# Performance work log

Hardware: AMD Instinct MI355X
Metric: run time of the kernel (lower is better)

## Reference

```python
import jax, jax.numpy as jnp
import numpy as np

EMBED = 1024
HEADS = 16
HEAD_DIM = EMBED // HEADS
WINDOW = 1024
HALF = WINDOW // 2  # effective causal lookback per token is HALF (window positions > i are masked)
SCALE = HEAD_DIM ** -0.5
B, T = 2, 4096


def setup_inputs() -> dict:
    key = jax.random.key(0)
    ks = jax.random.split(key, 11)
    f = jnp.float32
    return {
        'query': jax.random.normal(ks[0], (B, T, EMBED), f),
        'key':   jax.random.normal(ks[1], (B, T, EMBED), f),
        'value': jax.random.normal(ks[2], (B, T, EMBED), f),
        'wq': jax.random.normal(ks[3], (EMBED, EMBED), f) * 0.02,
        'bq': jax.random.normal(ks[4], (EMBED,), f) * 0.02,
        'wk': jax.random.normal(ks[5], (EMBED, EMBED), f) * 0.02,
        'bk': jax.random.normal(ks[6], (EMBED,), f) * 0.02,
        'wv': jax.random.normal(ks[7], (EMBED, EMBED), f) * 0.02,
        'bv': jax.random.normal(ks[8], (EMBED,), f) * 0.02,
        'wo': jax.random.normal(ks[9], (EMBED, EMBED), f) * 0.02,
        'bo': jax.random.normal(ks[10], (EMBED,), f) * 0.02,
    }


def _sliding_window_attn(q, k, v):
    # q,k,v: [B,H,T,D]; each query i attends to keys j with i-HALF <= j <= i.
    # Blocked formulation with block size Bk=HALF: block b attends to blocks b-1 and b.
    Bq, H, Tq, D = q.shape
    Bk = HALF
    nb = Tq // Bk  # T chosen to be a multiple of HALF
    qb = q.reshape(Bq, H, nb, Bk, D)

    def ctx(x):
        xb = x.reshape(Bq, H, nb, Bk, D)
        prev = jnp.concatenate([jnp.zeros_like(xb[:, :, :1]), xb[:, :, :-1]], axis=2)
        return jnp.concatenate([prev, xb], axis=3)  # [B,H,nb,2Bk,D]

    kc, vc = ctx(k), ctx(v)
    scores = jnp.einsum('bhnrd,bhncd->bhnrc', qb, kc)  # [B,H,nb,Bk,2Bk]
    r = jnp.arange(Bk)[:, None]          # query pos within block
    c = jnp.arange(2 * Bk)[None, :]      # key pos within [prev|cur] context
    # global diff = (Bk + r) - c; valid iff 0 <= diff <= HALF  <=>  r <= c <= r + Bk
    band = (c >= r) & (c <= r + Bk)      # [Bk, 2Bk]
    b_idx = jnp.arange(nb)[:, None, None]
    valid = band[None] & ((b_idx > 0) | (c[None] >= Bk))  # first block has no prev keys
    neg_inf = jnp.finfo(jnp.float32).min
    scores = jnp.where(valid[None, None], scores.astype(jnp.float32), neg_inf)
    attn = jax.nn.softmax(scores, axis=-1).astype(q.dtype)
    out = jnp.einsum('bhnrc,bhncd->bhnrd', attn, vc)
    return out.reshape(Bq, H, Tq, D)


def reference(query, key, value, wq, bq, wk, bk, wv, bv, wo, bo):
    Bq, Tq, C = query.shape
    split = lambda x: x.reshape(Bq, Tq, HEADS, HEAD_DIM).transpose(0, 2, 1, 3)
    q = split(jnp.einsum('btc,oc->bto', query, wq) + bq) * SCALE
    k = split(jnp.einsum('btc,oc->bto', key, wk) + bk)
    v = split(jnp.einsum('btc,oc->bto', value, wv) + bv)
    o = _sliding_window_attn(q, k, v)                       # [B,H,T,D]
    o = o.transpose(0, 2, 1, 3).reshape(Bq, Tq, C)
    return jnp.einsum('btc,oc->bto', o, wo) + bo
```

## Files before the change

### kernel.cpp

```cpp
#include <hip/hip_runtime.h>
#include <hip/hip_bf16.h>

typedef __attribute__((ext_vector_type(8))) short short8;
typedef __attribute__((ext_vector_type(4))) float f32x4;

__device__ __forceinline__ unsigned short f2bf(float f) {
  union { float f; unsigned int u; } x; x.f = f;
  unsigned int r = x.u + 0x7fffu + ((x.u >> 16) & 1u);
  return (unsigned short)(r >> 16);
}

__device__ __forceinline__ float fexp2(float x) {
#if __has_builtin(__builtin_amdgcn_exp2f)
  return __builtin_amdgcn_exp2f(x);
#else
  float r;
  asm("v_exp_f32 %0, %1" : "=v"(r) : "v"(x));
  return r;
#endif
}

#define MFMA16(a, b, c) __builtin_amdgcn_mfma_f32_16x16x32_bf16((a), (b), (c), 0, 0, 0)

__device__ __forceinline__ void gload_lds16(const void* g, void* l) {
  __builtin_amdgcn_global_load_lds((const __attribute__((address_space(1))) void*)g,
                                   (__attribute__((address_space(3))) void*)l, 16, 0, 0);
}

#define WAIT_VM(n) asm volatile("s_waitcnt vmcnt(" #n ")" ::: "memory")
#define RAW_BAR() asm volatile("s_barrier" ::: "memory")

__device__ __forceinline__ void p32swap(unsigned int& a, unsigned int& b) {
  asm volatile("v_permlane32_swap_b32 %0, %1" : "+v"(a), "+v"(b));
}
__device__ __forceinline__ void p16swap(unsigned int& a, unsigned int& b) {
  asm volatile("v_permlane16_swap_b32 %0, %1" : "+v"(a), "+v"(b));
}

#define QSCALE 0.1803368801111244f

__global__ __launch_bounds__(256) void cvt8(const float* __restrict__ in,
                                            unsigned short* __restrict__ out, int n8) {
  int i = blockIdx.x * 256 + threadIdx.x;
  if (i >= n8) return;
  const float4* p = (const float4*)in + 2 * (size_t)i;
  float4 a = p[0], b = p[1];
  ushort4 lo, hi;
  lo.x = f2bf(a.x); lo.y = f2bf(a.y); lo.z = f2bf(a.z); lo.w = f2bf(a.w);
  hi.x = f2bf(b.x); hi.y = f2bf(b.y); hi.z = f2bf(b.z); hi.w = f2bf(b.w);
  ((ushort4*)out)[2 * (size_t)i] = lo;
  ((ushort4*)out)[2 * (size_t)i + 1] = hi;
}

__global__ __launch_bounds__(256) void cvt_w(const float* __restrict__ w0,
                                             const float* __restrict__ w1,
                                             const float* __restrict__ w2,
                                             const float* __restrict__ w3,
                                             unsigned short* __restrict__ out) {
  const float* src = (blockIdx.y == 0) ? w0 : (blockIdx.y == 1) ? w1
                     : (blockIdx.y == 2) ? w2 : w3;
  unsigned short* o = out + ((size_t)blockIdx.y << 20);
  const int i = blockIdx.x * 256 + threadIdx.x;
  const float4* p = (const float4*)src + 2 * (size_t)i;
  float4 a = p[0], b = p[1];
  ushort4 lo, hi;
  lo.x = f2bf(a.x); lo.y = f2bf(a.y); lo.z = f2bf(a.z); lo.w = f2bf(a.w);
  hi.x = f2bf(b.x); hi.y = f2bf(b.y); hi.z = f2bf(b.z); hi.w = f2bf(b.w);
  ((ushort4*)o)[2 * (size_t)i] = lo;
  ((ushort4*)o)[2 * (size_t)i + 1] = hi;
}

template <int MODE>
__global__ __launch_bounds__(512) void proj_gemm(const unsigned short* __restrict__ A,
                                                 const unsigned short* __restrict__ W,
                                                 const float* __restrict__ bias,
                                                 void* __restrict__ outp) {
  __shared__ unsigned short As[2][128 * 64];
  __shared__ unsigned short Bs[2][128 * 64];
  const int tid = threadIdx.x, lane = tid & 63, wid = tid >> 6;
  const int g = lane >> 4, li = lane & 15;
  const int wr = wid >> 1, wc = wid & 1;
  const int bm = blockIdx.y, bn = blockIdx.x;
  const int trow = tid >> 3;
  const int js = (tid & 7) ^ (trow & 7);

  f32x4 acc[2][4] = {};

  auto stage = [&](int kt, int pb) {
    const int k0 = kt << 6;
    #pragma unroll
    for (int r = 0; r < 2; ++r) {
      const int row = r * 64 + trow;
      gload_lds16(A + (size_t)(bm * 128 + row) * 1024 + k0 + js * 8,
                  &As[pb][(r * 64 + wid * 8) * 64]);
      gload_lds16(W + (size_t)(bn * 128 + row) * 1024 + k0 + js * 8,
                  &Bs[pb][(r * 64 + wid * 8) * 64]);
    }
  };

  stage(0, 0);
  int p = 0;
  for (int kt = 0; kt < 16; ++kt) {
    if (kt < 15) {
      stage(kt + 1, p ^ 1);
      WAIT_VM(4);
    } else {
      WAIT_VM(0);
    }
    RAW_BAR();
    #pragma unroll
    for (int kst = 0; kst < 2; ++kst) {
      short8 a[2], b[4];
      #pragma unroll
      for (int mi = 0; mi < 2; ++mi) {
        const int row = wr * 32 + mi * 16 + li;
        a[mi] = *(const short8*)((const char*)&As[p][0] + row * 128 +
                                 (((kst * 4 + g) ^ (li & 7)) << 4));
      }
      #pragma unroll
      for (int ni = 0; ni < 4; ++ni) {
        const int row = wc * 64 + ni * 16 + li;
        b[ni] = *(const short8*)((const char*)&Bs[p][0] + row * 128 +
                                 (((kst * 4 + g) ^ (li & 7)) << 4));
      }
      __builtin_amdgcn_s_setprio(1);
      #pragma unroll
      for (int mi = 0; mi < 2; ++mi)
        #pragma unroll
        for (int ni = 0; ni < 4; ++ni) {
          if constexpr (MODE == 2)
            acc[mi][ni] = MFMA16(b[ni], a[mi], acc[mi][ni]);
          else
            acc[mi][ni] = MFMA16(a[mi], b[ni], acc[mi][ni]);
        }
      __builtin_amdgcn_s_setprio(0);
    }
    RAW_BAR();
    p ^= 1;
  }

  #pragma unroll
  for (int mi = 0; mi < 2; ++mi) {
    #pragma unroll
    for (int ni = 0; ni < 4; ++ni) {
      if constexpr (MODE == 2) {
        const int mm = bm * 128 + wr * 32 + mi * 16 + li;
        const int b_ = mm >> 12, t_ = mm & 4095;
        #pragma unroll
        for (int r = 0; r < 4; ++r) {
          const int nn = bn * 128 + wc * 64 + ni * 16 + g * 4 + r;
          const int h_ = nn >> 6, d_ = nn & 63;
          float v = acc[mi][ni][r] + bias[nn];
          ((unsigned short*)outp)[(((size_t)(b_ * 16 + h_) * 64 + d_) << 12) + t_] = f2bf(v);
        }
      } else {
        const int nn = bn * 128 + wc * 64 + ni * 16 + li;
        const float bv_ = bias[nn];
        #pragma unroll
        for (int r = 0; r < 4; ++r) {
          const int mm = bm * 128 + wr * 32 + mi * 16 + g * 4 + r;
          float v = acc[mi][ni][r] + bv_;
          if constexpr (MODE == 0) v *= QSCALE;
          if constexpr (MODE <= 1) {
            const int b_ = mm >> 12, t_ = mm & 4095, h_ = nn >> 6, d_ = nn & 63;
            ((unsigned short*)outp)[(((size_t)(b_ * 16 + h_) * 4096 + t_) << 6) + d_] = f2bf(v);
          } else {
            ((float*)outp)[(size_t)mm * 1024 + nn] = v;
          }
        }
      }
    }
  }
}

__global__ __launch_bounds__(256) void swa_attn(const unsigned short* __restrict__ Q,
                                                const unsigned short* __restrict__ K,
                                                const unsigned short* __restrict__ V,
                                                unsigned short* __restrict__ O) {
  __shared__ unsigned short Kb[2][4096];
  __shared__ unsigned short Vb[2][4096];
  const int tid = threadIdx.x, lane = tid & 63, w = tid >> 6;
  const int g = lane >> 4, li = lane & 15;
  const int qs = blockIdx.x << 7, h = blockIdx.y, b = blockIdx.z;
  const int bh = b * 16 + h;
  const unsigned short* Qh = Q + ((size_t)bh << 18);
  const unsigned short* Kh = K + ((size_t)bh << 18);
  const unsigned short* Vh = V + ((size_t)bh << 18);

  short8 qa[2][2];
  #pragma unroll
  for (int qt = 0; qt < 2; ++qt)
    #pragma unroll
    for (int kst = 0; kst < 2; ++kst)
      qa[qt][kst] =
          *(const short8*)&Qh[((size_t)(qs + w * 32 + qt * 16 + li) << 6) + kst * 32 + g * 8];

  const short8 vone = {0x3F80, 0x3F80, 0x3F80, 0x3F80, 0x3F80, 0x3F80, 0x3F80, 0x3F80};
  f32x4 o[2][4] = {};
  f32x4 lac[2] = {};
  const int c0 = (qs >= 512) ? 0 : ((512 - qs) >> 6);

  const int srow_hi = lane >> 3;
  const int sj = lane & 7;

  auto stage = [&](int c, int pb) {
    const int ks = qs - 512 + (c << 6);
    #pragma unroll
    for (int i = 0; i < 2; ++i) {
      const int seg = w + i * 4;
      const int row = seg * 8 + srow_hi;
      const int jsw = sj ^ (row & 7);
      gload_lds16(Kh + (((size_t)(ks + row)) << 6) + jsw * 8, &Kb[pb][seg * 512]);
      gload_lds16(Vh + (((size_t)row) << 12) + ks + jsw * 8, &Vb[pb][seg * 512]);
    }
  };

  int p = 0;
  stage(c0, 0);

  for (int c = c0; c <= 9; ++c) {
    if (c < 9) {
      stage(c + 1, p ^ 1);
      WAIT_VM(4);
    } else {
      WAIT_VM(0);
    }
    RAW_BAR();
    const int cb = c << 6;
    const bool anyq = (cb + 63 >= w * 32) && (cb <= w * 32 + 543);
    if (anyq) {
      short8 kf[4][2], vf[4][2];
      #pragma unroll
      for (int nt = 0; nt < 4; ++nt) {
        const int row = nt * 16 + li, rx = li & 7;
        #pragma unroll
        for (int kst = 0; kst < 2; ++kst) {
          const int byt = row * 128 + (((kst * 4 + g) ^ rx) << 4);
          kf[nt][kst] = *(const short8*)((const char*)&Kb[p][0] + byt);
          vf[nt][kst] = *(const short8*)((const char*)&Vb[p][0] + byt);
        }
      }
      #pragma unroll
      for (int qt = 0; qt < 2; ++qt) {
        const int base = w * 32 + qt * 16;
        if (cb + 63 < base || cb > base + 527) continue;
        f32x4 s[4];
        __builtin_amdgcn_s_setprio(1);
        #pragma unroll
        for (int nt = 0; nt < 4; ++nt) {
          f32x4 z = {};
          s[nt] = MFMA16(kf[nt][0], qa[qt][0], z);
          s[nt] = MFMA16(kf[nt][1], qa[qt][1], s[nt]);
        }
        __builtin_amdgcn_s_setprio(0);
        if (cb < base + 16 || cb + 63 > base + 512) {
          #pragma unroll
          for (int nt = 0; nt < 4; ++nt)
            #pragma unroll
            for (int r = 0; r < 4; ++r) {
              const int t1 = cb + nt * 16 + g * 4 + r - base;
              if (t1 < li || t1 > 512 + li) s[nt][r] = -3e38f;
            }
        }
        unsigned int pw[4][2];
        #pragma unroll
        for (int nt = 0; nt < 4; ++nt) {
          float2 ab; ab.x = fexp2(s[nt][0]); ab.y = fexp2(s[nt][1]);
          float2 cd; cd.x = fexp2(s[nt][2]); cd.y = fexp2(s[nt][3]);
          union { __hip_bfloat162 h2; unsigned int u; } u0, u1;
          u0.h2 = __float22bfloat162_rn(ab);
          u1.h2 = __float22bfloat162_rn(cd);
          pw[nt][0] = u0.u;
          pw[nt][1] = u1.u;
        }
        short8 pbf[2];
        #pragma unroll
        for (int kst = 0; kst < 2; ++kst) {
          unsigned int A0 = pw[2 * kst][0], B0 = pw[2 * kst + 1][0];
          unsigned int A1 = pw[2 * kst][1], B1 = pw[2 * kst + 1][1];
          p32swap(A0, B0);
          p32swap(A1, B1);
          p16swap(A0, B0);
          p16swap(A1, B1);
          union { unsigned int u[4]; short8 s8; } pb_;
          pb_.u[0] = A0;
          pb_.u[1] = A1;
          pb_.u[2] = B0;
          pb_.u[3] = B1;
          pbf[kst] = pb_.s8;
        }
        __builtin_amdgcn_s_setprio(1);
        lac[qt] = MFMA16(vone, pbf[0], lac[qt]);
        lac[qt] = MFMA16(vone, pbf[1], lac[qt]);
        #pragma unroll
        for (int dt = 0; dt < 4; ++dt) {
          o[qt][dt] = MFMA16(vf[dt][0], pbf[0], o[qt][dt]);
          o[qt][dt] = MFMA16(vf[dt][1], pbf[1], o[qt][dt]);
        }
        __builtin_amdgcn_s_setprio(0);
      }
    }
    RAW_BAR();
    p ^= 1;
  }

  #pragma unroll
  for (int qt = 0; qt < 2; ++qt) {
    const float inv = 1.0f / lac[qt][0];
    const int t_ = qs + w * 32 + qt * 16 + li;
    #pragma unroll
    for (int dt = 0; dt < 4; ++dt) {
      ushort4 u;
      u.x = f2bf(o[qt][dt][0] * inv); u.y = f2bf(o[qt][dt][1] * inv);
      u.z = f2bf(o[qt][dt][2] * inv); u.w = f2bf(o[qt][dt][3] * inv);
      *(ushort4*)&O[((size_t)(b * 4096 + t_) << 10) + h * 64 + dt * 16 + g * 4] = u;
    }
  }
}

extern "C" void kernel_launch(void* const* d_in, const int* in_sizes, int n_in,
                              void* d_out, int out_size, void* d_ws, size_t ws_size,
                              hipStream_t stream) {
  const float* q_in = (const float*)d_in[0];
  const float* k_in = (const float*)d_in[1];
  const float* v_in = (const float*)d_in[2];
  const float* wq = (const float*)d_in[3];
  const float* bq = (const float*)d_in[4];
  const float* wk = (const float*)d_in[5];
  const float* bk = (const float*)d_in[6];
  const float* wv = (const float*)d_in[7];
  const float* bv = (const float*)d_in[8];
  const float* wo = (const float*)d_in[9];
  const float* bo = (const float*)d_in[10];

  unsigned short* Qw = (unsigned short*)d_ws;
  unsigned short* Kw = Qw + (size_t)8388608;
  unsigned short* Vw = Kw + (size_t)8388608;
  unsigned short* Tb = Vw + (size_t)8388608;
  unsigned short* Wb = Tb + (size_t)8388608;

  dim3 bb(256), bg(512), gg(8, 64);
  cvt_w<<<dim3(512, 4), bb, 0, stream>>>(wq, wk, wv, wo, Wb);
  cvt8<<<4096, bb, 0, stream>>>(q_in, Tb, 1048576);
  proj_gemm<0><<<gg, bg, 0, stream>>>(Tb, Wb, bq, Qw);
  cvt8<<<4096, bb, 0, stream>>>(k_in, Tb, 1048576);
  proj_gemm<1><<<gg, bg, 0, stream>>>(Tb, Wb + (1u << 20), bk, Kw);
  cvt8<<<4096, bb, 0, stream>>>(v_in, Tb, 1048576);
  proj_gemm<2><<<gg, bg, 0, stream>>>(Tb, Wb + (2u << 20), bv, Vw);
  swa_attn<<<dim3(32, 16, 2), bb, 0, stream>>>(Qw, Kw, Vw, Tb);
  proj_gemm<3><<<gg, bg, 0, stream>>>(Tb, Wb + (3u << 20), bo, (float*)d_out);
}
```

Before: 182.9 us.

## Fuse all fp32-to-bf16 conversions into one launch and remap grids for locality

Merges the weight and three activation conversion kernels into a single launch, storing converted K and V in the output buffer as scratch so all conversions can run up front. Swaps the GEMM grid so the M tile varies fastest, and remaps attention blocks so neighbouring query blocks of the same head land on the same XCD for L2 reuse of K/V. This cuts launch count and inter-kernel gaps, at the risk of different cache behaviour for the GEMM weight tiles.

```diff
diff --git a/kernel.cpp b/kernel.cpp
--- a/kernel.cpp
+++ b/kernel.cpp
@@ -39,35 +39,32 @@
 
 #define QSCALE 0.1803368801111244f
 
-__global__ __launch_bounds__(256) void cvt8(const float* __restrict__ in,
-                                            unsigned short* __restrict__ out, int n8) {
-  int i = blockIdx.x * 256 + threadIdx.x;
-  if (i >= n8) return;
-  const float4* p = (const float4*)in + 2 * (size_t)i;
+__global__ __launch_bounds__(256) void cvt_all(
+    const float* __restrict__ q, const float* __restrict__ k,
+    const float* __restrict__ v, const float* __restrict__ w0,
+    const float* __restrict__ w1, const float* __restrict__ w2,
+    const float* __restrict__ w3, unsigned short* __restrict__ Tb,
+    unsigned short* __restrict__ Kc, unsigned short* __restrict__ Vc,
+    unsigned short* __restrict__ Wb) {
+  const int lin = blockIdx.x;
+  const float* src;
+  unsigned short* dst;
+  int i0;
+  if (lin < 4096)        { src = q;  dst = Tb;                i0 = lin; }
+  else if (lin < 8192)   { src = k;  dst = Kc;                i0 = lin - 4096; }
+  else if (lin < 12288)  { src = v;  dst = Vc;                i0 = lin - 8192; }
+  else if (lin < 12800)  { src = w0; dst = Wb;                i0 = lin - 12288; }
+  else if (lin < 13312)  { src = w1; dst = Wb + (1u << 20);   i0 = lin - 12800; }
+  else if (lin < 13824)  { src = w2; dst = Wb + (2u << 20);   i0 = lin - 13312; }
+  else                   { src = w3; dst = Wb + (3u << 20);   i0 = lin - 13824; }
+  const size_t i = (size_t)i0 * 256 + threadIdx.x;
+  const float4* p = (const float4*)src + 2 * i;
   float4 a = p[0], b = p[1];
   ushort4 lo, hi;
   lo.x = f2bf(a.x); lo.y = f2bf(a.y); lo.z = f2bf(a.z); lo.w = f2bf(a.w);
   hi.x = f2bf(b.x); hi.y = f2bf(b.y); hi.z = f2bf(b.z); hi.w = f2bf(b.w);
-  ((ushort4*)out)[2 * (size_t)i] = lo;
-  ((ushort4*)out)[2 * (size_t)i + 1] = hi;
-}
-
-__global__ __launch_bounds__(256) void cvt_w(const float* __restrict__ w0,
-                                             const float* __restrict__ w1,
-                                             const float* __restrict__ w2,
-                                             const float* __restrict__ w3,
-                                             unsigned short* __restrict__ out) {
-  const float* src = (blockIdx.y == 0) ? w0 : (blockIdx.y == 1) ? w1
-                     : (blockIdx.y == 2) ? w2 : w3;
-  unsigned short* o = out + ((size_t)blockIdx.y << 20);
-  const int i = blockIdx.x * 256 + threadIdx.x;
-  const float4* p = (const float4*)src + 2 * (size_t)i;
-  float4 a = p[0], b = p[1];
-  ushort4 lo, hi;
-  lo.x = f2bf(a.x); lo.y = f2bf(a.y); lo.z = f2bf(a.z); lo.w = f2bf(a.w);
-  hi.x = f2bf(b.x); hi.y = f2bf(b.y); hi.z = f2bf(b.z); hi.w = f2bf(b.w);
-  ((ushort4*)o)[2 * (size_t)i] = lo;
-  ((ushort4*)o)[2 * (size_t)i + 1] = hi;
+  ((ushort4*)dst)[2 * i] = lo;
+  ((ushort4*)dst)[2 * i + 1] = hi;
 }
 
 template <int MODE>
@@ -80,7 +77,7 @@
   const int tid = threadIdx.x, lane = tid & 63, wid = tid >> 6;
   const int g = lane >> 4, li = lane & 15;
   const int wr = wid >> 1, wc = wid & 1;
-  const int bm = blockIdx.y, bn = blockIdx.x;
+  const int bm = blockIdx.x, bn = blockIdx.y;
   const int trow = tid >> 3;
   const int js = (tid & 7) ^ (trow & 7);
 
@@ -181,7 +178,16 @@
   __shared__ unsigned short Vb[2][4096];
   const int tid = threadIdx.x, lane = tid & 63, w = tid >> 6;
   const int g = lane >> 4, li = lane & 15;
-  const int qs = blockIdx.x << 7, h = blockIdx.y, b = blockIdx.z;
+  const int lin = blockIdx.x;
+  const int xcd = lin & 7;
+  const int rest = lin >> 3;
+  const int qoff = rest & 7;
+  const int grp = rest >> 3;
+  const int G = xcd * 16 + grp;
+  const int hb = G & 31;
+  const int qb = (G >> 5) * 8 + qoff;
+  const int qs = qb << 7;
+  const int h = hb & 15, b = hb >> 4;
   const int bh = b * 16 + h;
   const unsigned short* Qh = Q + ((size_t)bh << 18);
   const unsigned short* Kh = K + ((size_t)bh << 18);
@@ -338,15 +344,15 @@
   unsigned short* Vw = Kw + (size_t)8388608;
   unsigned short* Tb = Vw + (size_t)8388608;
   unsigned short* Wb = Tb + (size_t)8388608;
-
-  dim3 bb(256), bg(512), gg(8, 64);
-  cvt_w<<<dim3(512, 4), bb, 0, stream>>>(wq, wk, wv, wo, Wb);
-  cvt8<<<4096, bb, 0, stream>>>(q_in, Tb, 1048576);
+  unsigned short* Kc = (unsigned short*)d_out;
+  unsigned short* Vc = Kc + (size_t)8388608;
+
+  dim3 bb(256), bg(512), gg(64, 8);
+  cvt_all<<<14336, bb, 0, stream>>>(q_in, k_in, v_in, wq, wk, wv, wo,
+                                    Tb, Kc, Vc, Wb);
   proj_gemm<0><<<gg, bg, 0, stream>>>(Tb, Wb, bq, Qw);
-  cvt8<<<4096, bb, 0, stream>>>(k_in, Tb, 1048576);
-  proj_gemm<1><<<gg, bg, 0, stream>>>(Tb, Wb + (1u << 20), bk, Kw);
-  cvt8<<<4096, bb, 0, stream>>>(v_in, Tb, 1048576);
-  proj_gemm<2><<<gg, bg, 0, stream>>>(Tb, Wb + (2u << 20), bv, Vw);
-  swa_attn<<<dim3(32, 16, 2), bb, 0, stream>>>(Qw, Kw, Vw, Tb);
+  proj_gemm<1><<<gg, bg, 0, stream>>>(Kc, Wb + (1u << 20), bk, Kw);
+  proj_gemm<2><<<gg, bg, 0, stream>>>(Vc, Wb + (2u << 20), bv, Vw);
+  swa_attn<<<1024, bb, 0, stream>>>(Qw, Kw, Vw, Tb);
   proj_gemm<3><<<gg, bg, 0, stream>>>(Tb, Wb + (3u << 20), bo, (float*)d_out);
 }
```

Result: faster. 157.8 us (-13.7%).
